# Kernel tuning notes

Hardware: AMD Instinct MI355X
Metric: run time of the kernel (lower is better)

Reference implementation:

```python
import jax, jax.numpy as jnp
import numpy as np
import math

EMBED_DIM = 1024
NUM_HEADS = 16
HEAD_DIM = EMBED_DIM // NUM_HEADS


def setup_inputs() -> dict:
    key = jax.random.key(0)
    ks = jax.random.split(key, 12)
    B, N = 2, 2048
    s = 1.0 / math.sqrt(EMBED_DIM)
    inp = {
        "query": jax.random.normal(ks[0], (B, N, EMBED_DIM), jnp.float32),
        "key": jax.random.normal(ks[1], (B, N, EMBED_DIM), jnp.float32),
        "value": jax.random.normal(ks[2], (B, N, EMBED_DIM), jnp.float32),
        "Wq": jax.random.normal(ks[3], (EMBED_DIM, EMBED_DIM), jnp.float32) * s,
        "bq": jnp.zeros((EMBED_DIM,), jnp.float32),
        "Wk": jax.random.normal(ks[4], (EMBED_DIM, EMBED_DIM), jnp.float32) * s,
        "bk": jnp.zeros((EMBED_DIM,), jnp.float32),
        "Wv": jax.random.normal(ks[5], (EMBED_DIM, EMBED_DIM), jnp.float32) * s,
        "bv": jnp.zeros((EMBED_DIM,), jnp.float32),
        "Wo": jax.random.normal(ks[6], (EMBED_DIM, EMBED_DIM), jnp.float32) * s,
        "bo": jnp.zeros((EMBED_DIM,), jnp.float32),
        "gate": jnp.zeros((NUM_HEADS,), jnp.float32),
    }
    return inp


def reference(query, key, value, Wq, bq, Wk, bk, Wv, bv, Wo, bo, gate):
    B, Nq, _ = query.shape
    Nk = key.shape[1]
    H, D = NUM_HEADS, HEAD_DIM
    # projections (Linear: x @ W.T + b); split heads -> [B, H, N, D]
    q = (query @ Wq.T + bq).reshape(B, Nq, H, D).transpose(0, 2, 1, 3)
    k = (key @ Wk.T + bk).reshape(B, Nk, H, D).transpose(0, 2, 1, 3)
    v = (value @ Wv.T + bv).reshape(B, Nk, H, D).transpose(0, 2, 1, 3)
    # scaled logits with per-head sigmoid gate folded into the scale
    scale = jax.nn.sigmoid(gate) / math.sqrt(D)  # [H]
    logits = jnp.einsum("bhqd,bhkd->bhqk", q, k) * scale[None, :, None, None]
    attn = jax.nn.softmax(logits, axis=-1)
    out = jnp.einsum("bhqk,bhkd->bhqd", attn, v)
    out = out.transpose(0, 2, 1, 3).reshape(B, Nq, H * D)
    return out @ Wo.T + bo
```

## Files before the change

### kernel.cpp

```cpp
#include <hip/hip_runtime.h>
#include <hip/hip_bf16.h>
#include <cstdint>


#define DEV __device__ __forceinline__
typedef __attribute__((ext_vector_type(8))) short bf16x8;
typedef __attribute__((ext_vector_type(4))) float f32x4;
typedef unsigned short u16;

DEV void async16(const void* g, void* l) {
  __builtin_amdgcn_global_load_lds(
      (const __attribute__((address_space(1))) unsigned int*)g,
      (__attribute__((address_space(3))) unsigned int*)l, 16, 0, 0);
}

DEV u16 bf16_rne(float f) {
  unsigned int u = __builtin_bit_cast(unsigned int, f);
  u += 0x7FFFu + ((u >> 16) & 1u);
  return (u16)(u >> 16);
}

DEV u16 cvt16(float x) {
  __hip_bfloat16 h = __float2bfloat16(x);
  return __builtin_bit_cast(u16, h);
}

DEV unsigned cvtpk(float lo, float hi) {
  unsigned r;
  asm("v_cvt_pk_bf16_f32 %0, %1, %2" : "=v"(r) : "v"(lo), "v"(hi));
  return r;
}

DEV uint4 cvt8(float4 a, float4 b) {
  union { u16 us[8]; uint4 v; } u;
  u.us[0] = bf16_rne(a.x); u.us[1] = bf16_rne(a.y);
  u.us[2] = bf16_rne(a.z); u.us[3] = bf16_rne(a.w);
  u.us[4] = bf16_rne(b.x); u.us[5] = bf16_rne(b.y);
  u.us[6] = bf16_rne(b.z); u.us[7] = bf16_rne(b.w);
  return u.v;
}

__global__ __launch_bounds__(256) void cast_w(
    const float* __restrict__ Wq, const float* __restrict__ Wk,
    const float* __restrict__ Wv, const float* __restrict__ Wo,
    u16* __restrict__ WQB, u16* __restrict__ WKB, u16* __restrict__ WVB,
    u16* __restrict__ WOB) {
  int idx = blockIdx.x * 256 + threadIdx.x;
  const float* src; u16* dst; int i;
  if      (idx < 131072) { src = Wq; dst = WQB; i = idx; }
  else if (idx < 262144) { src = Wk; dst = WKB; i = idx - 131072; }
  else if (idx < 393216) { src = Wv; dst = WVB; i = idx - 262144; }
  else                   { src = Wo; dst = WOB; i = idx - 393216; }
  const float4* p = (const float4*)src + (size_t)i * 2;
  ((uint4*)dst)[i] = cvt8(p[0], p[1]);
}

__global__ __launch_bounds__(256, 3) void gemm_qkv(
    const float* __restrict__ Xq, const float* __restrict__ Xk, const float* __restrict__ Xv,
    const u16* __restrict__ Wb,
    const float* __restrict__ bq, const float* __restrict__ bkb, const float* __restrict__ bv,
    const float* __restrict__ gate,
    u16* __restrict__ QB, u16* __restrict__ KB, u16* __restrict__ VTB) {
  __shared__ __attribute__((aligned(16))) u16 As[2][128 * 32];
  __shared__ __attribute__((aligned(16))) u16 Bs[2][128 * 32];
  const int t = threadIdx.x, lane = t & 63, w = t >> 6;
  const int l15 = lane & 15, quad = lane >> 4;
  const int xcd = blockIdx.x & 7, idx = blockIdx.x >> 3;
  const int seg = idx >> 5, r5 = idx & 31;
  const int bm = (xcd << 2) + (r5 >> 3), bn = r5 & 7;
  const int m0 = bm << 7, n0 = bn << 7;
  const float* A = (seg == 0) ? Xq : (seg == 1) ? Xk : Xv;
  const u16* W = Wb + (long)seg * 1048576;
  const int wm = (w >> 1) << 6, wn = (w & 1) << 6;
  const int r0 = t >> 2, cc0 = (t & 3) * 8;
  const float* gA0 = A + (long)(m0 + r0) * 1024 + cc0;
  const float* gA1 = gA0 + 64 * 1024;
  const u16* gB0 = W + (long)(n0 + r0) * 1024 + cc0;
  const u16* gB1 = gB0 + 64 * 1024;

  float4 ra0, ra1, ra2, ra3;
  auto LOADA = [&](int ko) {
    const float4* p0 = (const float4*)(gA0 + ko);
    const float4* p1 = (const float4*)(gA1 + ko);
    ra0 = p0[0]; ra1 = p0[1]; ra2 = p1[0]; ra3 = p1[1];
  };
  auto WRITEA = [&](int nb) {
    *(uint4*)&As[nb][t * 8] = cvt8(ra0, ra1);
    *(uint4*)&As[nb][(t + 256) * 8] = cvt8(ra2, ra3);
  };

  LOADA(0);
  async16(gB0, &Bs[0][t * 8]); async16(gB1, &Bs[0][(t + 256) * 8]);
  WRITEA(0);
  LOADA(32);

  f32x4 acc[4][4] = {};
  for (int k0 = 0; k0 < 1024; k0 += 32) {
    const int cur = (k0 >> 5) & 1;
    __syncthreads();
    if (k0 + 32 < 1024) {
      const int kn = k0 + 32, nb = cur ^ 1;
      WRITEA(nb);
      async16(gB0 + kn, &Bs[nb][t * 8]); async16(gB1 + kn, &Bs[nb][(t + 256) * 8]);
      if (k0 + 64 < 1024) LOADA(k0 + 64);
    }
    bf16x8 af[4], bfm[4];
#pragma unroll
    for (int i = 0; i < 4; i++)
      af[i] = *(const bf16x8*)&As[cur][(wm + i * 16 + l15) * 32 + quad * 8];
#pragma unroll
    for (int j = 0; j < 4; j++)
      bfm[j] = *(const bf16x8*)&Bs[cur][(wn + j * 16 + l15) * 32 + quad * 8];
#pragma unroll
    for (int i = 0; i < 4; i++)
#pragma unroll
      for (int j = 0; j < 4; j++)
        acc[i][j] = __builtin_amdgcn_mfma_f32_16x16x32_bf16(af[i], bfm[j], acc[i][j], 0, 0, 0);
  }

  if (seg == 2) {
#pragma unroll
    for (int i = 0; i < 4; i++) {
      int token = m0 + wm + i * 16 + quad * 4;
      int bb_ = token >> 11, n = token & 2047;
#pragma unroll
      for (int j = 0; j < 4; j++) {
        int col = n0 + wn + j * 16 + l15;
        float bb = bv[col];
        union { u16 us[4]; uint2 u2; } pk;
#pragma unroll
        for (int r = 0; r < 4; r++) pk.us[r] = bf16_rne(acc[i][j][r] + bb);
        *(uint2*)&VTB[(long)(bb_ * 1024 + col) * 2048 + n] = pk.u2;
      }
    }
  } else {
    const float* bias = seg ? bkb : bq;
    u16* C = seg ? KB : QB;
#pragma unroll
    for (int j = 0; j < 4; j++) {
      int col = n0 + wn + j * 16 + l15;
      float bb = bias[col];
      float scl = 1.f;
      if (seg == 0) {
        float g = gate[col >> 6];
        float sig = 1.f / (1.f + __builtin_amdgcn_exp2f(-g * 1.44269504f));
        scl = sig * 0.125f * 1.44269504f;
      }
#pragma unroll
      for (int i = 0; i < 4; i++) {
        int row = m0 + wm + i * 16 + quad * 4;
#pragma unroll
        for (int r = 0; r < 4; r++)
          C[(long)(row + r) * 1024 + col] = bf16_rne((acc[i][j][r] + bb) * scl);
      }
    }
  }
}

__global__ __launch_bounds__(256, 4) void gemm_out(
    const u16* __restrict__ A, const u16* __restrict__ W,
    const float* __restrict__ bias, float* __restrict__ Cf) {
  __shared__ __attribute__((aligned(16))) u16 As[2][64 * 32];
  __shared__ __attribute__((aligned(16))) u16 Bs[2][64 * 32];
  const int t = threadIdx.x, lane = t & 63, w = t >> 6;
  const int l15 = lane & 15, quad = lane >> 4;
  const int xcd = blockIdx.x & 7, idx = blockIdx.x >> 3;
  const int bm = (xcd << 3) + (idx >> 4), bn = idx & 15;
  const int m0 = bm << 6, n0 = bn << 6;
  const int wm = (w >> 1) << 5, wn = (w & 1) << 5;
  const int r0 = t >> 2, cc0 = (t & 3) * 8;
  const u16* gA = A + (long)(m0 + r0) * 1024 + cc0;
  const u16* gB = W + (long)(n0 + r0) * 1024 + cc0;

  async16(gA, &As[0][t * 8]);
  async16(gB, &Bs[0][t * 8]);

  f32x4 acc[2][2] = {};
  for (int k0 = 0; k0 < 1024; k0 += 32) {
    const int cur = (k0 >> 5) & 1;
    __syncthreads();
    if (k0 + 32 < 1024) {
      const int kn = k0 + 32, nb = cur ^ 1;
      async16(gA + kn, &As[nb][t * 8]);
      async16(gB + kn, &Bs[nb][t * 8]);
    }
    bf16x8 af[2], bfm[2];
#pragma unroll
    for (int i = 0; i < 2; i++)
      af[i] = *(const bf16x8*)&As[cur][(wm + i * 16 + l15) * 32 + quad * 8];
#pragma unroll
    for (int j = 0; j < 2; j++)
      bfm[j] = *(const bf16x8*)&Bs[cur][(wn + j * 16 + l15) * 32 + quad * 8];
#pragma unroll
    for (int i = 0; i < 2; i++)
#pragma unroll
      for (int j = 0; j < 2; j++)
        acc[i][j] = __builtin_amdgcn_mfma_f32_16x16x32_bf16(af[i], bfm[j], acc[i][j], 0, 0, 0);
  }

#pragma unroll
  for (int j = 0; j < 2; j++) {
    int col = n0 + wn + j * 16 + l15;
    float bb = bias[col];
#pragma unroll
    for (int i = 0; i < 2; i++) {
      int row = m0 + wm + i * 16 + quad * 4;
#pragma unroll
      for (int r = 0; r < 4; r++)
        Cf[(long)(row + r) * 1024 + col] = acc[i][j][r] + bb;
    }
  }
}

__global__ __launch_bounds__(256, 4) void attn_kernel(
    const u16* __restrict__ Q, const u16* __restrict__ Kb,
    const u16* __restrict__ Vt, u16* __restrict__ Op0, u16* __restrict__ Op3,
    float* __restrict__ lp) {
  __shared__ __attribute__((aligned(16))) u16 Ks[2][32 * 64];
  __shared__ __attribute__((aligned(16))) u16 Vs[2][64 * 32];
  const int t = threadIdx.x, lane = t & 63, w = t >> 6;
  const int l15 = lane & 15, quad = lane >> 4;
  const int xcd = blockIdx.x & 7, rr = blockIdx.x >> 3;
  const int ksp = xcd >> 1, qt = ((xcd & 1) << 3) | rr;
  const int h = blockIdx.y, b = blockIdx.z;
  const int q0 = qt * 128, tok0 = b * 2048, key0 = ksp * 512;
  const u16* Kbase = Kb + (long)tok0 * 1024 + h * 64;
  const u16* Vbase = Vt + (long)(b * 1024 + h * 64) * 2048 + key0;

  bf16x8 aq[2][2];
#pragma unroll
  for (int i = 0; i < 2; i++) {
    long row = tok0 + q0 + w * 32 + i * 16 + l15;
#pragma unroll
    for (int ks = 0; ks < 2; ks++)
      aq[i][ks] = *(const bf16x8*)&Q[row * 1024 + h * 64 + ks * 32 + quad * 8];
  }

  const int rk = t >> 3, ck = t & 7;
  const int rv = t >> 2, cv = t & 3;
  const u16* kg = Kbase + (long)(key0 + rk) * 1024 + ((ck ^ ((rk >> 1) & 7)) * 8);
  const u16* vg = Vbase + (long)rv * 2048 + ((cv ^ ((rv >> 1) & 3)) * 8);
  u16* ksd = &Ks[0][t * 8];
  u16* vsd = &Vs[0][t * 8];

  auto STAGE = [&](int tk, int bu) {
    async16(kg + (long)tk * 32768, ksd + bu * 2048);
    async16(vg + tk * 32, vsd + bu * 2048);
  };

  STAGE(0, 0);

  float l_st[2] = {};
  f32x4 O[2][4] = {};

  for (int kt = 0; kt < 16; kt++) {
    const int cur = kt & 1;
    __syncthreads();
    if (kt + 1 < 16) STAGE(kt + 1, cur ^ 1);

    f32x4 s[2][2] = {};
    __builtin_amdgcn_s_setprio(1);
#pragma unroll
    for (int ks = 0; ks < 2; ks++) {
      bf16x8 bk_[2];
#pragma unroll
      for (int j = 0; j < 2; j++) {
        int rl = 2 * l15 + j;
        bk_[j] = *(const bf16x8*)&Ks[cur][rl * 64 + (((ks * 4 + quad) ^ (l15 & 7))) * 8];
      }
#pragma unroll
      for (int i = 0; i < 2; i++)
#pragma unroll
        for (int j = 0; j < 2; j++)
          s[i][j] = __builtin_amdgcn_mfma_f32_16x16x32_bf16(bk_[j], aq[i][ks], s[i][j], 0, 0, 0);
    }
    __builtin_amdgcn_s_setprio(0);

    bf16x8 ap[2];
#pragma unroll
    for (int i = 0; i < 2; i++) {
      union { unsigned uw[4]; bf16x8 v8; } pw;
#pragma unroll
      for (int r = 0; r < 4; r++) {
        float p0 = __builtin_amdgcn_exp2f(s[i][0][r]);
        float p1 = __builtin_amdgcn_exp2f(s[i][1][r]);
        l_st[i] += p0 + p1;
        pw.uw[r] = cvtpk(p0, p1);
      }
      ap[i] = pw.v8;
    }

    bf16x8 bv_[4];
#pragma unroll
    for (int dj = 0; dj < 4; dj++) {
      int rl = dj * 16 + l15;
      bv_[dj] = *(const bf16x8*)&Vs[cur][rl * 32 + ((quad ^ ((rl >> 1) & 3))) * 8];
    }
    __builtin_amdgcn_s_setprio(1);
#pragma unroll
    for (int i = 0; i < 2; i++)
#pragma unroll
      for (int dj = 0; dj < 4; dj++)
        O[i][dj] = __builtin_amdgcn_mfma_f32_16x16x32_bf16(ap[i], bv_[dj], O[i][dj], 0, 0, 0);
    __builtin_amdgcn_s_setprio(0);
  }

  u16* dst = (ksp == 3) ? Op3 : (Op0 + (long)ksp * 4194304);
#pragma unroll
  for (int i = 0; i < 2; i++) {
    float ls = l_st[i];
    ls += __shfl_xor(ls, 16); ls += __shfl_xor(ls, 32);
    if (quad == 0) {
      long qrow = tok0 + q0 + w * 32 + i * 16 + l15;
      lp[ksp * 65536 + (int)qrow * 16 + h] = ls;
    }
#pragma unroll
    for (int r = 0; r < 4; r++) {
      long row = tok0 + q0 + w * 32 + i * 16 + quad * 4 + r;
#pragma unroll
      for (int dj = 0; dj < 4; dj++)
        dst[row * 1024 + h * 64 + dj * 16 + l15] = cvt16(O[i][dj][r]);
    }
  }
}

__global__ __launch_bounds__(256) void merge_kernel(
    const u16* __restrict__ Op0, const u16* __restrict__ Op3,
    const float* __restrict__ lp, u16* __restrict__ AO) {
  int idx = blockIdx.x * 256 + threadIdx.x;
  int tok = idx >> 7, rem = idx & 127, h = rem >> 3;
  int li = tok * 16 + h;
  float inv = 1.f / (lp[li] + lp[65536 + li] + lp[131072 + li] + lp[196608 + li]);
  union U { uint4 v; u16 us[8]; };
  U a0, a1, a2, a3, uo;
  a0.v = ((const uint4*)Op0)[idx];
  a1.v = ((const uint4*)Op0)[idx + 524288];
  a2.v = ((const uint4*)Op0)[idx + 1048576];
  a3.v = ((const uint4*)Op3)[idx];
#pragma unroll
  for (int j = 0; j < 8; j++) {
    float f0 = __builtin_bit_cast(float, (unsigned)((unsigned)a0.us[j] << 16));
    float f1 = __builtin_bit_cast(float, (unsigned)((unsigned)a1.us[j] << 16));
    float f2 = __builtin_bit_cast(float, (unsigned)((unsigned)a2.us[j] << 16));
    float f3 = __builtin_bit_cast(float, (unsigned)((unsigned)a3.us[j] << 16));
    uo.us[j] = cvt16((f0 + f1 + f2 + f3) * inv);
  }
  ((uint4*)AO)[idx] = uo.v;
}

extern "C" void kernel_launch(void* const* d_in, const int* in_sizes, int n_in,
                              void* d_out, int out_size, void* d_ws, size_t ws_size,
                              hipStream_t stream) {
  const float* q  = (const float*)d_in[0];
  const float* k  = (const float*)d_in[1];
  const float* v  = (const float*)d_in[2];
  const float* Wq = (const float*)d_in[3];
  const float* bq = (const float*)d_in[4];
  const float* Wk = (const float*)d_in[5];
  const float* bk = (const float*)d_in[6];
  const float* Wv = (const float*)d_in[7];
  const float* bv = (const float*)d_in[8];
  const float* Wo = (const float*)d_in[9];
  const float* bo = (const float*)d_in[10];
  const float* gate = (const float*)d_in[11];
  float* out = (float*)d_out;
  char* ws = (char*)d_ws;

  const size_t MB = 1u << 20;
  u16* WQB = (u16*)(ws + 0 * MB);
  u16* WKB = (u16*)(ws + 2 * MB);
  u16* WVB = (u16*)(ws + 4 * MB);
  u16* WOB = (u16*)(ws + 6 * MB);
  u16* QB  = (u16*)(ws + 32 * MB);
  u16* KB  = (u16*)(ws + 40 * MB);
  u16* OPp  = (u16*)(ws + 8 * MB);
  u16* OPd3 = (u16*)((char*)d_out + 8 * MB);
  float* LP = (float*)(ws + 0 * MB);
  u16* AOB  = (u16*)(ws + 8 * MB);
  u16* VTB  = (u16*)d_out;

  cast_w<<<2048, 256, 0, stream>>>(Wq, Wk, Wv, Wo, WQB, WKB, WVB, WOB);
  gemm_qkv<<<768, 256, 0, stream>>>(q, k, v, WQB, bq, bk, bv, gate, QB, KB, VTB);
  attn_kernel<<<dim3(64, 16, 2), 256, 0, stream>>>(QB, KB, VTB, OPp, OPd3, LP);
  merge_kernel<<<2048, 256, 0, stream>>>(OPp, OPd3, LP, AOB);
  gemm_out<<<1024, 256, 0, stream>>>(AOB, WOB, bo, out);
}
```

Baseline: 227.1 us.

## Fuse weight fp32-to-bf16 casting into GEMM loaders and drop cast kernel

Removes the separate cast_w kernel and has gemm_qkv and gemm_out load the fp32 weights directly, converting them to bf16 in registers before writing to LDS. gemm_qkv's N tile shrinks from 128 to 64, doubling the grid and raising the occupancy hint to 5. cvt8 now uses packed v_cvt_pk_bf16_f32 instructions instead of manual rounding. This saves a launch and a round trip of the weights through memory, but each GEMM tile now reads fp32 weights (twice the bytes) and A tiles are reloaded more often with the narrower N tile.

```diff
diff --git a/kernel.cpp b/kernel.cpp
--- a/kernel.cpp
+++ b/kernel.cpp
@@ -32,89 +32,78 @@
 }
 
 DEV uint4 cvt8(float4 a, float4 b) {
-  union { u16 us[8]; uint4 v; } u;
-  u.us[0] = bf16_rne(a.x); u.us[1] = bf16_rne(a.y);
-  u.us[2] = bf16_rne(a.z); u.us[3] = bf16_rne(a.w);
-  u.us[4] = bf16_rne(b.x); u.us[5] = bf16_rne(b.y);
-  u.us[6] = bf16_rne(b.z); u.us[7] = bf16_rne(b.w);
-  return u.v;
-}
-
-__global__ __launch_bounds__(256) void cast_w(
-    const float* __restrict__ Wq, const float* __restrict__ Wk,
-    const float* __restrict__ Wv, const float* __restrict__ Wo,
-    u16* __restrict__ WQB, u16* __restrict__ WKB, u16* __restrict__ WVB,
-    u16* __restrict__ WOB) {
-  int idx = blockIdx.x * 256 + threadIdx.x;
-  const float* src; u16* dst; int i;
-  if      (idx < 131072) { src = Wq; dst = WQB; i = idx; }
-  else if (idx < 262144) { src = Wk; dst = WKB; i = idx - 131072; }
-  else if (idx < 393216) { src = Wv; dst = WVB; i = idx - 262144; }
-  else                   { src = Wo; dst = WOB; i = idx - 393216; }
-  const float4* p = (const float4*)src + (size_t)i * 2;
-  ((uint4*)dst)[i] = cvt8(p[0], p[1]);
-}
-
-__global__ __launch_bounds__(256, 3) void gemm_qkv(
+  uint4 v;
+  v.x = cvtpk(a.x, a.y);
+  v.y = cvtpk(a.z, a.w);
+  v.z = cvtpk(b.x, b.y);
+  v.w = cvtpk(b.z, b.w);
+  return v;
+}
+
+__global__ __launch_bounds__(256, 5) void gemm_qkv(
     const float* __restrict__ Xq, const float* __restrict__ Xk, const float* __restrict__ Xv,
-    const u16* __restrict__ Wb,
+    const float* __restrict__ Wqf, const float* __restrict__ Wkf, const float* __restrict__ Wvf,
     const float* __restrict__ bq, const float* __restrict__ bkb, const float* __restrict__ bv,
     const float* __restrict__ gate,
     u16* __restrict__ QB, u16* __restrict__ KB, u16* __restrict__ VTB) {
   __shared__ __attribute__((aligned(16))) u16 As[2][128 * 32];
-  __shared__ __attribute__((aligned(16))) u16 Bs[2][128 * 32];
+  __shared__ __attribute__((aligned(16))) u16 Bs[2][64 * 32];
   const int t = threadIdx.x, lane = t & 63, w = t >> 6;
   const int l15 = lane & 15, quad = lane >> 4;
   const int xcd = blockIdx.x & 7, idx = blockIdx.x >> 3;
-  const int seg = idx >> 5, r5 = idx & 31;
-  const int bm = (xcd << 2) + (r5 >> 3), bn = r5 & 7;
-  const int m0 = bm << 7, n0 = bn << 7;
+  const int seg = idx >> 6, r6 = idx & 63;
+  const int bm = (xcd << 2) + (r6 >> 4), bn = r6 & 15;
+  const int m0 = bm << 7, n0 = bn << 6;
   const float* A = (seg == 0) ? Xq : (seg == 1) ? Xk : Xv;
-  const u16* W = Wb + (long)seg * 1048576;
-  const int wm = (w >> 1) << 6, wn = (w & 1) << 6;
+  const float* W = (seg == 0) ? Wqf : (seg == 1) ? Wkf : Wvf;
+  const int wm = (w >> 1) << 6, wn = (w & 1) << 5;
   const int r0 = t >> 2, cc0 = (t & 3) * 8;
   const float* gA0 = A + (long)(m0 + r0) * 1024 + cc0;
   const float* gA1 = gA0 + 64 * 1024;
-  const u16* gB0 = W + (long)(n0 + r0) * 1024 + cc0;
-  const u16* gB1 = gB0 + 64 * 1024;
-
-  float4 ra0, ra1, ra2, ra3;
+  const float* gB = W + (long)(n0 + r0) * 1024 + cc0;
+
+  float4 ra0, ra1, ra2, ra3, rb0, rb1;
   auto LOADA = [&](int ko) {
     const float4* p0 = (const float4*)(gA0 + ko);
     const float4* p1 = (const float4*)(gA1 + ko);
     ra0 = p0[0]; ra1 = p0[1]; ra2 = p1[0]; ra3 = p1[1];
   };
+  auto LOADB = [&](int ko) {
+    const float4* p = (const float4*)(gB + ko);
+    rb0 = p[0]; rb1 = p[1];
+  };
   auto WRITEA = [&](int nb) {
     *(uint4*)&As[nb][t * 8] = cvt8(ra0, ra1);
     *(uint4*)&As[nb][(t + 256) * 8] = cvt8(ra2, ra3);
   };
-
-  LOADA(0);
-  async16(gB0, &Bs[0][t * 8]); async16(gB1, &Bs[0][(t + 256) * 8]);
-  WRITEA(0);
-  LOADA(32);
-
-  f32x4 acc[4][4] = {};
+  auto WRITEB = [&](int nb) {
+    *(uint4*)&Bs[nb][t * 8] = cvt8(rb0, rb1);
+  };
+
+  LOADA(0); LOADB(0);
+  WRITEA(0); WRITEB(0);
+  LOADA(32); LOADB(32);
+
+  f32x4 acc[4][2] = {};
   for (int k0 = 0; k0 < 1024; k0 += 32) {
     const int cur = (k0 >> 5) & 1;
     __syncthreads();
     if (k0 + 32 < 1024) {
-      const int kn = k0 + 32, nb = cur ^ 1;
-      WRITEA(nb);
-      async16(gB0 + kn, &Bs[nb][t * 8]); async16(gB1 + kn, &Bs[nb][(t + 256) * 8]);
-      if (k0 + 64 < 1024) LOADA(k0 + 64);
-    }
-    bf16x8 af[4], bfm[4];
+      const int nb = cur ^ 1;
+      WRITEA(nb); WRITEB(nb);
+      if (k0 + 64 < 1024) { LOADA(k0 + 64); LOADB(k0 + 64); }
+    }
+    bf16x8 af[4], bfm[2];
 #pragma unroll
     for (int i = 0; i < 4; i++)
       af[i] = *(const bf16x8*)&As[cur][(wm + i * 16 + l15) * 32 + quad * 8];
 #pragma unroll
-    for (int j = 0; j < 4; j++)
+    for (int j = 0; j < 2; j++)
       bfm[j] = *(const bf16x8*)&Bs[cur][(wn + j * 16 + l15) * 32 + quad * 8];
 #pragma unroll
     for (int i = 0; i < 4; i++)
 #pragma unroll
-      for (int j = 0; j < 4; j++)
+      for (int j = 0; j < 2; j++)
         acc[i][j] = __builtin_amdgcn_mfma_f32_16x16x32_bf16(af[i], bfm[j], acc[i][j], 0, 0, 0);
   }
 
@@ -124,7 +113,7 @@
       int token = m0 + wm + i * 16 + quad * 4;
       int bb_ = token >> 11, n = token & 2047;
 #pragma unroll
-      for (int j = 0; j < 4; j++) {
+      for (int j = 0; j < 2; j++) {
         int col = n0 + wn + j * 16 + l15;
         float bb = bv[col];
         union { u16 us[4]; uint2 u2; } pk;
@@ -137,7 +126,7 @@
     const float* bias = seg ? bkb : bq;
     u16* C = seg ? KB : QB;
 #pragma unroll
-    for (int j = 0; j < 4; j++) {
+    for (int j = 0; j < 2; j++) {
       int col = n0 + wn + j * 16 + l15;
       float bb = bias[col];
       float scl = 1.f;
@@ -158,7 +147,7 @@
 }
 
 __global__ __launch_bounds__(256, 4) void gemm_out(
-    const u16* __restrict__ A, const u16* __restrict__ W,
+    const u16* __restrict__ A, const float* __restrict__ Wof,
     const float* __restrict__ bias, float* __restrict__ Cf) {
   __shared__ __attribute__((aligned(16))) u16 As[2][64 * 32];
   __shared__ __attribute__((aligned(16))) u16 Bs[2][64 * 32];
@@ -170,10 +159,19 @@
   const int wm = (w >> 1) << 5, wn = (w & 1) << 5;
   const int r0 = t >> 2, cc0 = (t & 3) * 8;
   const u16* gA = A + (long)(m0 + r0) * 1024 + cc0;
-  const u16* gB = W + (long)(n0 + r0) * 1024 + cc0;
+  const float* gB = Wof + (long)(n0 + r0) * 1024 + cc0;
+
+  float4 rb0, rb1;
+  auto LOADB = [&](int ko) {
+    const float4* p = (const float4*)(gB + ko);
+    rb0 = p[0]; rb1 = p[1];
+  };
+  auto WRITEB = [&](int nb) {
+    *(uint4*)&Bs[nb][t * 8] = cvt8(rb0, rb1);
+  };
 
   async16(gA, &As[0][t * 8]);
-  async16(gB, &Bs[0][t * 8]);
+  LOADB(0); WRITEB(0); LOADB(32);
 
   f32x4 acc[2][2] = {};
   for (int k0 = 0; k0 < 1024; k0 += 32) {
@@ -182,7 +180,8 @@
     if (k0 + 32 < 1024) {
       const int kn = k0 + 32, nb = cur ^ 1;
       async16(gA + kn, &As[nb][t * 8]);
-      async16(gB + kn, &Bs[nb][t * 8]);
+      WRITEB(nb);
+      if (k0 + 64 < 1024) LOADB(k0 + 64);
     }
     bf16x8 af[2], bfm[2];
 #pragma unroll
@@ -367,10 +366,6 @@
   char* ws = (char*)d_ws;
 
   const size_t MB = 1u << 20;
-  u16* WQB = (u16*)(ws + 0 * MB);
-  u16* WKB = (u16*)(ws + 2 * MB);
-  u16* WVB = (u16*)(ws + 4 * MB);
-  u16* WOB = (u16*)(ws + 6 * MB);
   u16* QB  = (u16*)(ws + 32 * MB);
   u16* KB  = (u16*)(ws + 40 * MB);
   u16* OPp  = (u16*)(ws + 8 * MB);
@@ -379,9 +374,9 @@
   u16* AOB  = (u16*)(ws + 8 * MB);
   u16* VTB  = (u16*)d_out;
 
-  cast_w<<<2048, 256, 0, stream>>>(Wq, Wk, Wv, Wo, WQB, WKB, WVB, WOB);
-  gemm_qkv<<<768, 256, 0, stream>>>(q, k, v, WQB, bq, bk, bv, gate, QB, KB, VTB);
+  gemm_qkv<<<1536, 256, 0, stream>>>(q, k, v, Wq, Wk, Wv, bq, bk, bv, gate,
+                                     QB, KB, VTB);
   attn_kernel<<<dim3(64, 16, 2), 256, 0, stream>>>(QB, KB, VTB, OPp, OPd3, LP);
   merge_kernel<<<2048, 256, 0, stream>>>(OPp, OPd3, LP, AOB);
-  gemm_out<<<1024, 256, 0, stream>>>(AOB, WOB, bo, out);
-}
+  gemm_out<<<1024, 256, 0, stream>>>(AOB, Wo, bo, out);
+}
```

After: 252.6 us. 11.2% more time.
